# Kernel tuning notes

Hardware: AMD Instinct MI355X
Metric: run time of the kernel (lower is better)

The kernel has to match this reference:

```python
import jax, jax.numpy as jnp
import numpy as np

K = 8
W_CONST = 0.01
EPS = 1e-8


def _normalize(v, eps=1e-8):
    return v / (jnp.linalg.norm(v, axis=-1, keepdims=True) + eps)


def _coarse_normal(x, vertices, vertex_normals):
    # x: (N,3); vertices, vertex_normals: (V,3)
    # brute-force KNN (ascending by squared distance, like cKDTree.query)
    d2_all = jnp.sum((x[:, None, :] - vertices[None, :, :]) ** 2, axis=-1)  # (N,V)
    neg_d2, idx = jax.lax.top_k(-d2_all, K)  # sorted ascending distance
    d2 = -neg_d2                                                    # (N,K)
    v_knn = vertices[idx]                                           # (N,K,3)
    n_knn = vertex_normals[idx]                                     # (N,K,3)
    d2c = jnp.maximum(d2, EPS)
    inv_d2 = 1.0 / d2c                                              # (N,K)
    term_knn = jnp.sum(n_knn * inv_d2[..., None], axis=1)           # (N,3)
    v1 = v_knn[:, 0]                                                # nearest vertex
    d2_v1 = jnp.maximum(jnp.sum((x - v1) ** 2, axis=-1), EPS)       # (N,)
    term_dir = (x - v1) / (W_CONST * d2_v1[:, None])
    W = jnp.sum(inv_d2, axis=1) + 1.0 / W_CONST                     # (N,)
    n_tilde = (term_knn + term_dir) / W[:, None]
    nc = _normalize(n_tilde)
    return nc, v1


def _ray_mesh_first_hit(origins, dirs, tri0, e1, e2):
    # Moller-Trumbore, all points vs all faces. origins/dirs: (N,3); tri0/e1/e2: (F,3)
    pvec = jnp.cross(dirs[:, None, :], e2[None, :, :])              # (N,F,3)
    det = jnp.einsum('fk,nfk->nf', e1, pvec)                        # (N,F)
    ok_det = jnp.abs(det) > EPS
    inv_det = jnp.where(ok_det, 1.0 / jnp.where(ok_det, det, 1.0), 0.0)
    tvec = origins[:, None, :] - tri0[None, :, :]                   # (N,F,3)
    u = jnp.sum(tvec * pvec, axis=-1) * inv_det
    qvec = jnp.cross(tvec, e1[None, :, :])                          # (N,F,3)
    v = jnp.einsum('nk,nfk->nf', dirs, qvec) * inv_det
    t = jnp.einsum('fk,nfk->nf', e2, qvec) * inv_det
    valid = ok_det & (u >= 0.0) & (v >= 0.0) & (u + v <= 1.0) & (t > EPS)
    t_masked = jnp.where(valid, t, jnp.inf)
    t_min = jnp.min(t_masked, axis=1)                               # first hit along ray
    hit = jnp.isfinite(t_min)
    loc = origins + dirs * jnp.where(hit, t_min, 0.0)[:, None]
    return hit, loc


def _project(x, vertices, vertex_normals, faces):
    nc, v1 = _coarse_normal(x, vertices, vertex_normals)
    tri0 = vertices[faces[:, 0]]
    e1 = vertices[faces[:, 1]] - tri0
    e2 = vertices[faces[:, 2]] - tri0
    # primary cast along -nc
    hit1, loc1 = _ray_mesh_first_hit(x, -nc, tri0, e1, e2)
    # fallback cast toward nearest vertex
    dir_fb = _normalize(v1 - x)
    hit2, loc2 = _ray_mesh_first_hit(x, dir_fb, tri0, e1, e2)
    xc = jnp.where(hit1[:, None], loc1, jnp.where(hit2[:, None], loc2, v1))
    s = jnp.sum((x - xc) * nc, axis=-1, keepdims=True)              # (N,1)
    return xc, s, nc


def setup_inputs() -> dict:
    key = jax.random.key(0)
    k1, k2, k3, k4 = jax.random.split(key, 4)
    N, V, F = 2048, 8192, 8192
    x = jax.random.normal(k1, (N, 3), dtype=jnp.float32)
    vertices = jax.random.normal(k2, (V, 3), dtype=jnp.float32)
    vertex_normals = _normalize(jax.random.normal(k3, (V, 3), dtype=jnp.float32))
    faces = jax.random.randint(k4, (F, 3), 0, V, dtype=jnp.int32)
    return {"x": x, "vertices": vertices, "vertex_normals": vertex_normals, "faces": faces}


def reference(x, vertices, vertex_normals, faces):
    # returns (xc:(N,3), s:(N,1), nc:(N,3)) like ProjectionFn.forward
    return _project(x, vertices, vertex_normals, faces)
```

## Files before the change

### kernel.cpp

```cpp
#include <hip/hip_runtime.h>
#include <math.h>

#pragma float_control(precise, on)

#define EPSF 1e-8f


__global__ void __launch_bounds__(256) knn_prep_kernel(
    const float* __restrict__ x, const float* __restrict__ verts,
    const float* __restrict__ vnorm, const int* __restrict__ faces,
    float* __restrict__ tri, float* __restrict__ ncw,
    float* __restrict__ v1w, float* __restrict__ dfbw,
    int N, int V, int F) {
#pragma clang fp contract(off)
    int p = blockIdx.x;
    int tid = threadIdx.x;
    int wave = tid >> 6;
    int lane = tid & 63;
    if (p >= N) return;

    int gt = p * 256 + tid;
    if (gt < F) {
        int f0 = faces[gt * 3 + 0];
        int f1 = faces[gt * 3 + 1];
        int f2 = faces[gt * 3 + 2];
        float t0x = verts[f0 * 3 + 0], t0y = verts[f0 * 3 + 1], t0z = verts[f0 * 3 + 2];
        float ax = verts[f1 * 3 + 0], ay = verts[f1 * 3 + 1], az = verts[f1 * 3 + 2];
        float bx = verts[f2 * 3 + 0], by = verts[f2 * 3 + 1], bz = verts[f2 * 3 + 2];
        float4* t4 = (float4*)(tri + (size_t)gt * 12);
        t4[0] = make_float4(t0x, t0y, t0z, ax - t0x);
        t4[1] = make_float4(ay - t0y, az - t0z, bx - t0x, by - t0y);
        t4[2] = make_float4(bz - t0z, 0.f, 0.f, 0.f);
    }

    float xx = x[p * 3 + 0];
    float xy = x[p * 3 + 1];
    float xz = x[p * 3 + 2];

    unsigned long long ka[8], kb[8];
#pragma unroll
    for (int i = 0; i < 8; ++i) { ka[i] = ~0ULL; kb[i] = ~0ULL; }

    for (int va = tid; va < V; va += 512) {
        int vb = va + 256;
        bool hasB = vb < V;

        float avx = verts[va * 3 + 0];
        float avy = verts[va * 3 + 1];
        float avz = verts[va * 3 + 2];
        float bvx = 0.f, bvy = 0.f, bvz = 0.f;
        if (hasB) {
            bvx = verts[vb * 3 + 0];
            bvy = verts[vb * 3 + 1];
            bvz = verts[vb * 3 + 2];
        }

        float dxa = xx - avx, dya = xy - avy, dza = xz - avz;
        float d2a = ((dxa * dxa) + (dya * dya)) + (dza * dza);
        unsigned long long kA =
            (((unsigned long long)__float_as_uint(d2a)) << 32) | (unsigned int)va;
        if (kA < ka[7]) {
            ka[7] = kA;
#pragma unroll
            for (int j = 7; j > 0; --j) {
                if (ka[j] < ka[j - 1]) {
                    unsigned long long t = ka[j];
                    ka[j] = ka[j - 1];
                    ka[j - 1] = t;
                }
            }
        }

        if (hasB) {
            float dxb = xx - bvx, dyb = xy - bvy, dzb = xz - bvz;
            float d2b = ((dxb * dxb) + (dyb * dyb)) + (dzb * dzb);
            unsigned long long kB =
                (((unsigned long long)__float_as_uint(d2b)) << 32) | (unsigned int)vb;
            if (kB < kb[7]) {
                kb[7] = kB;
#pragma unroll
                for (int j = 7; j > 0; --j) {
                    if (kb[j] < kb[j - 1]) {
                        unsigned long long t = kb[j];
                        kb[j] = kb[j - 1];
                        kb[j - 1] = t;
                    }
                }
            }
        }
    }

    unsigned long long wsel[8];
#pragma unroll
    for (int j = 0; j < 8; ++j) {
        unsigned long long c = (ka[0] < kb[0]) ? ka[0] : kb[0];
        unsigned long long m = c;
#pragma unroll
        for (int s = 1; s < 64; s <<= 1) {
            unsigned long long o = __shfl_xor(m, s, 64);
            if (o < m) m = o;
        }
        if (c == m) {
            if (ka[0] == m) {
#pragma unroll
                for (int t = 0; t < 7; ++t) ka[t] = ka[t + 1];
                ka[7] = ~0ULL;
            } else {
#pragma unroll
                for (int t = 0; t < 7; ++t) kb[t] = kb[t + 1];
                kb[7] = ~0ULL;
            }
        }
        wsel[j] = m;
    }

    __shared__ unsigned long long cand[32];
    if (lane == 0) {
#pragma unroll
        for (int j = 0; j < 8; ++j) cand[wave * 8 + j] = wsel[j];
    }
    __syncthreads();
    if (wave != 0) return;

    unsigned long long c0 = (lane < 32) ? cand[lane] : ~0ULL;
    unsigned long long sel[8];
#pragma unroll
    for (int j = 0; j < 8; ++j) {
        unsigned long long m = c0;
#pragma unroll
        for (int s = 1; s < 64; s <<= 1) {
            unsigned long long o = __shfl_xor(m, s, 64);
            if (o < m) m = o;
        }
        if (c0 == m) c0 = ~0ULL;
        sel[j] = m;
    }

    if (lane != 0) return;

    float invk[8];
    float nsx = 0.f, nsy = 0.f, nsz = 0.f;
#pragma unroll
    for (int j = 0; j < 8; ++j) {
        int id = (int)(sel[j] & 0xffffffffu);
        float d2 = __uint_as_float((unsigned int)(sel[j] >> 32));
        float inv = 1.0f / fmaxf(d2, EPSF);
        invk[j] = inv;
        nsx = nsx + vnorm[id * 3 + 0] * inv;
        nsy = nsy + vnorm[id * 3 + 1] * inv;
        nsz = nsz + vnorm[id * 3 + 2] * inv;
    }
    float Wsum = ((invk[0] + invk[1]) + (invk[2] + invk[3])) +
                 ((invk[4] + invk[5]) + (invk[6] + invk[7]));

    int id0 = (int)(sel[0] & 0xffffffffu);
    float v1x = verts[id0 * 3 + 0];
    float v1y = verts[id0 * 3 + 1];
    float v1z = verts[id0 * 3 + 2];

    float dxv = xx - v1x, dyv = xy - v1y, dzv = xz - v1z;
    float d2v1 = fmaxf(((dxv * dxv) + (dyv * dyv)) + (dzv * dzv), EPSF);
    float den = 0.01f * d2v1;
    float tdx = dxv / den, tdy = dyv / den, tdz = dzv / den;

    float W = Wsum + 100.0f;
    float ntx = (nsx + tdx) / W;
    float nty = (nsy + tdy) / W;
    float ntz = (nsz + tdz) / W;
    float nrm = sqrtf(((ntx * ntx) + (nty * nty)) + (ntz * ntz)) + 1e-8f;
    float ncx = ntx / nrm, ncy = nty / nrm, ncz = ntz / nrm;

    float fx = v1x - xx, fy = v1y - xy, fz = v1z - xz;
    float fn = sqrtf(((fx * fx) + (fy * fy)) + (fz * fz)) + 1e-8f;
    fx = fx / fn; fy = fy / fn; fz = fz / fn;

    ncw[p * 3 + 0] = ncx; ncw[p * 3 + 1] = ncy; ncw[p * 3 + 2] = ncz;
    v1w[p * 3 + 0] = v1x; v1w[p * 3 + 1] = v1y; v1w[p * 3 + 2] = v1z;
    dfbw[p * 3 + 0] = fx; dfbw[p * 3 + 1] = fy; dfbw[p * 3 + 2] = fz;
}

__device__ __forceinline__ float mt_test(
    float ox, float oy, float oz, float dx, float dy, float dz,
    const float4 A, const float4 B, const float4 C, float tb) {
#pragma clang fp contract(off)
    const float M = 1e-5f;
    float e1x = A.w, e1y = B.x, e1z = B.y;
    float e2x = B.z, e2y = B.w, e2z = C.x;
    float tvx = ox - A.x;
    float tvy = oy - A.y;
    float tvz = oz - A.z;
    float qx = (tvy * e1z) - (tvz * e1y);
    float qy = (tvz * e1x) - (tvx * e1z);
    float qz = (tvx * e1y) - (tvy * e1x);
    float tq = ((e2x * qx) + (e2y * qy)) + (e2z * qz);
    float px = (dy * e2z) - (dz * e2y);
    float py = (dz * e2x) - (dx * e2z);
    float pz = (dx * e2y) - (dy * e2x);
    float det = ((e1x * px) + (e1y * py)) + (e1z * pz);
    bool ok = fabsf(det) > EPSF;
    float inv = ok ? (1.0f / det) : 0.0f;
    float u = (((tvx * px) + (tvy * py)) + (tvz * pz)) * inv;
    float v = (((dx * qx) + (dy * qy)) + (dz * qz)) * inv;
    float t = tq * inv;
    bool valid = ok && (u >= -M) && (v >= -M) && ((u + v) <= 1.0f + M) && (t > EPSF);
    return (valid && t < tb) ? t : tb;
}

__global__ void __launch_bounds__(512) ray_fin_kernel(
    const float* __restrict__ x, const float* __restrict__ tri,
    const float* __restrict__ ncw, const float* __restrict__ v1w,
    const float* __restrict__ dfbw, float* __restrict__ out, int N, int F) {
#pragma clang fp contract(off)
    __shared__ unsigned int redA[8], redB[8];
    __shared__ unsigned int u1As, u1Bs, u2As, u2Bs, hAf, hBf;
    int b = blockIdx.x;
    int tid = threadIdx.x;
    int wave = tid >> 6;
    int lane = tid & 63;
    int pA = 2 * b;
    if (pA >= N) return;
    int pB = pA + 1;
    bool hasB = pB < N;
    int pBs = hasB ? pB : pA;

    float axx = x[pA * 3 + 0], axy = x[pA * 3 + 1], axz = x[pA * 3 + 2];
    float Ancx = ncw[pA * 3 + 0], Ancy = ncw[pA * 3 + 1], Ancz = ncw[pA * 3 + 2];
    float Adbx = dfbw[pA * 3 + 0], Adby = dfbw[pA * 3 + 1], Adbz = dfbw[pA * 3 + 2];
    float Adax = -Ancx, Aday = -Ancy, Adaz = -Ancz;

    float bxx = x[pBs * 3 + 0], bxy = x[pBs * 3 + 1], bxz = x[pBs * 3 + 2];
    float Bncx = ncw[pBs * 3 + 0], Bncy = ncw[pBs * 3 + 1], Bncz = ncw[pBs * 3 + 2];
    float Bdbx = dfbw[pBs * 3 + 0], Bdby = dfbw[pBs * 3 + 1], Bdbz = dfbw[pBs * 3 + 2];
    float Bdax = -Bncx, Bday = -Bncy, Bdaz = -Bncz;

    const float INF = __uint_as_float(0x7f800000u);

    float tA = INF, tB = INF;
    for (int fi = tid; fi < F; fi += 512) {
        const float4 A4 = *(const float4*)(tri + (size_t)fi * 12);
        const float4 B4 = *(const float4*)(tri + (size_t)fi * 12 + 4);
        const float4 C4 = *(const float4*)(tri + (size_t)fi * 12 + 8);
        tA = mt_test(axx, axy, axz, Adax, Aday, Adaz, A4, B4, C4, tA);
        tB = mt_test(bxx, bxy, bxz, Bdax, Bday, Bdaz, A4, B4, C4, tB);
    }

    {
        unsigned int ma = __float_as_uint(tA);
        unsigned int mb = __float_as_uint(tB);
#pragma unroll
        for (int s = 1; s < 64; s <<= 1) {
            unsigned int oa = __shfl_xor(ma, s, 64);
            if (oa < ma) ma = oa;
            unsigned int ob = __shfl_xor(mb, s, 64);
            if (ob < mb) mb = ob;
        }
        if (lane == 0) { redA[wave] = ma; redB[wave] = mb; }
    }
    __syncthreads();
    if (tid == 0) {
        unsigned int u1A = min(min(min(redA[0], redA[1]), min(redA[2], redA[3])),
                               min(min(redA[4], redA[5]), min(redA[6], redA[7])));
        unsigned int u1B = min(min(min(redB[0], redB[1]), min(redB[2], redB[3])),
                               min(min(redB[4], redB[5]), min(redB[6], redB[7])));
        u1As = u1A; u1Bs = u1B;
        hAf = (u1A < 0x7f800000u) ? 1u : 0u;
        hBf = (u1B < 0x7f800000u) ? 1u : 0u;
    }
    __syncthreads();

    bool needA = (hAf == 0u);
    bool needB = hasB && (hBf == 0u);
    if (needA || needB) {
        float sA = INF, sB = INF;
        for (int fi = tid; fi < F; fi += 512) {
            const float4 A4 = *(const float4*)(tri + (size_t)fi * 12);
            const float4 B4 = *(const float4*)(tri + (size_t)fi * 12 + 4);
            const float4 C4 = *(const float4*)(tri + (size_t)fi * 12 + 8);
            if (needA) sA = mt_test(axx, axy, axz, Adbx, Adby, Adbz, A4, B4, C4, sA);
            if (needB) sB = mt_test(bxx, bxy, bxz, Bdbx, Bdby, Bdbz, A4, B4, C4, sB);
        }
        unsigned int ma = __float_as_uint(sA);
        unsigned int mb = __float_as_uint(sB);
#pragma unroll
        for (int s = 1; s < 64; s <<= 1) {
            unsigned int oa = __shfl_xor(ma, s, 64);
            if (oa < ma) ma = oa;
            unsigned int ob = __shfl_xor(mb, s, 64);
            if (ob < mb) mb = ob;
        }
        if (lane == 0) { redA[wave] = ma; redB[wave] = mb; }
        __syncthreads();
        if (tid == 0) {
            u2As = min(min(min(redA[0], redA[1]), min(redA[2], redA[3])),
                       min(min(redA[4], redA[5]), min(redA[6], redA[7])));
            u2Bs = min(min(min(redB[0], redB[1]), min(redB[2], redB[3])),
                       min(min(redB[4], redB[5]), min(redB[6], redB[7])));
        }
    }

    if (tid != 0) return;
    {
        float t1 = __uint_as_float(u1As);
        bool h1 = t1 < INF;
        float t2 = h1 ? INF : __uint_as_float(u2As);
        bool h2 = t2 < INF;
        float xcx, xcy, xcz;
        if (h1) {
            xcx = axx + ((-Ancx) * t1);
            xcy = axy + ((-Ancy) * t1);
            xcz = axz + ((-Ancz) * t1);
        } else if (h2) {
            xcx = axx + (Adbx * t2);
            xcy = axy + (Adby * t2);
            xcz = axz + (Adbz * t2);
        } else {
            xcx = v1w[pA * 3 + 0]; xcy = v1w[pA * 3 + 1]; xcz = v1w[pA * 3 + 2];
        }
        float s = (((axx - xcx) * Ancx) + ((axy - xcy) * Ancy)) + ((axz - xcz) * Ancz);
        out[pA * 3 + 0] = xcx;
        out[pA * 3 + 1] = xcy;
        out[pA * 3 + 2] = xcz;
        out[3 * N + pA] = s;
        out[4 * N + pA * 3 + 0] = Ancx;
        out[4 * N + pA * 3 + 1] = Ancy;
        out[4 * N + pA * 3 + 2] = Ancz;
    }
    if (hasB) {
        float t1 = __uint_as_float(u1Bs);
        bool h1 = t1 < INF;
        float t2 = h1 ? INF : __uint_as_float(u2Bs);
        bool h2 = t2 < INF;
        float xcx, xcy, xcz;
        if (h1) {
            xcx = bxx + ((-Bncx) * t1);
            xcy = bxy + ((-Bncy) * t1);
            xcz = bxz + ((-Bncz) * t1);
        } else if (h2) {
            xcx = bxx + (Bdbx * t2);
            xcy = bxy + (Bdby * t2);
            xcz = bxz + (Bdbz * t2);
        } else {
            xcx = v1w[pB * 3 + 0]; xcy = v1w[pB * 3 + 1]; xcz = v1w[pB * 3 + 2];
        }
        float s = (((bxx - xcx) * Bncx) + ((bxy - xcy) * Bncy)) + ((bxz - xcz) * Bncz);
        out[pB * 3 + 0] = xcx;
        out[pB * 3 + 1] = xcy;
        out[pB * 3 + 2] = xcz;
        out[3 * N + pB] = s;
        out[4 * N + pB * 3 + 0] = Bncx;
        out[4 * N + pB * 3 + 1] = Bncy;
        out[4 * N + pB * 3 + 2] = Bncz;
    }
}

extern "C" void kernel_launch(void* const* d_in, const int* in_sizes, int n_in,
                              void* d_out, int out_size, void* d_ws, size_t ws_size,
                              hipStream_t stream) {
    const float* x     = (const float*)d_in[0];
    const float* verts = (const float*)d_in[1];
    const float* vnorm = (const float*)d_in[2];
    const int*   faces = (const int*)d_in[3];
    int N = in_sizes[0] / 3;
    int V = in_sizes[1] / 3;
    int F = in_sizes[3] / 3;

    float* tri  = (float*)d_ws;
    float* ncw  = tri + (size_t)F * 12;
    float* v1w  = ncw + 3 * N;
    float* dfbw = v1w + 3 * N;

    hipLaunchKernelGGL(knn_prep_kernel, dim3(N), dim3(256), 0, stream,
                       x, verts, vnorm, faces, tri, ncw, v1w, dfbw, N, V, F);
    int rblocks = (N + 1) / 2;
    hipLaunchKernelGGL(ray_fin_kernel, dim3(rblocks), dim3(512), 0, stream,
                       x, tri, ncw, v1w, dfbw, (float*)d_out, N, F);
}
```

Measured before the change: 133.4 us.

## Process two query points per KNN block to share vertex loads

The KNN kernel now handles two query points per 512-thread block. Each vertex is loaded once and compared against both points, so each thread keeps two top-8 lists. This halves the global vertex traffic per query and halves the block count, but each thread does two insertions per vertex and the merge now has 8 waves. Triangle precompute becomes a grid-strided loop.

```diff
diff --git a/kernel.cpp b/kernel.cpp
--- a/kernel.cpp
+++ b/kernel.cpp
@@ -6,21 +6,24 @@
 #define EPSF 1e-8f
 
 
-__global__ void __launch_bounds__(256) knn_prep_kernel(
+__global__ void __launch_bounds__(512) knn_prep_kernel(
     const float* __restrict__ x, const float* __restrict__ verts,
     const float* __restrict__ vnorm, const int* __restrict__ faces,
     float* __restrict__ tri, float* __restrict__ ncw,
     float* __restrict__ v1w, float* __restrict__ dfbw,
     int N, int V, int F) {
 #pragma clang fp contract(off)
-    int p = blockIdx.x;
+    int b = blockIdx.x;
     int tid = threadIdx.x;
     int wave = tid >> 6;
     int lane = tid & 63;
-    if (p >= N) return;
-
-    int gt = p * 256 + tid;
-    if (gt < F) {
+    int pA = 2 * b;
+    if (pA >= N) return;
+    int pB = pA + 1;
+    bool hasB = pB < N;
+    int pBs = hasB ? pB : pA;
+
+    for (int gt = b * 512 + tid; gt < F; gt += gridDim.x * 512) {
         int f0 = faces[gt * 3 + 0];
         int f1 = faces[gt * 3 + 1];
         int f2 = faces[gt * 3 + 2];
@@ -33,110 +36,99 @@
         t4[2] = make_float4(bz - t0z, 0.f, 0.f, 0.f);
     }
 
-    float xx = x[p * 3 + 0];
-    float xy = x[p * 3 + 1];
-    float xz = x[p * 3 + 2];
-
-    unsigned long long ka[8], kb[8];
-#pragma unroll
-    for (int i = 0; i < 8; ++i) { ka[i] = ~0ULL; kb[i] = ~0ULL; }
-
-    for (int va = tid; va < V; va += 512) {
-        int vb = va + 256;
-        bool hasB = vb < V;
-
-        float avx = verts[va * 3 + 0];
-        float avy = verts[va * 3 + 1];
-        float avz = verts[va * 3 + 2];
-        float bvx = 0.f, bvy = 0.f, bvz = 0.f;
-        if (hasB) {
-            bvx = verts[vb * 3 + 0];
-            bvy = verts[vb * 3 + 1];
-            bvz = verts[vb * 3 + 2];
-        }
-
-        float dxa = xx - avx, dya = xy - avy, dza = xz - avz;
+    float axx = x[pA * 3 + 0], axy = x[pA * 3 + 1], axz = x[pA * 3 + 2];
+    float bxx = x[pBs * 3 + 0], bxy = x[pBs * 3 + 1], bxz = x[pBs * 3 + 2];
+
+    unsigned long long la[8], lb[8];
+#pragma unroll
+    for (int i = 0; i < 8; ++i) { la[i] = ~0ULL; lb[i] = ~0ULL; }
+
+    for (int v = tid; v < V; v += 512) {
+        float vx = verts[v * 3 + 0];
+        float vy = verts[v * 3 + 1];
+        float vz = verts[v * 3 + 2];
+
+        float dxa = axx - vx, dya = axy - vy, dza = axz - vz;
         float d2a = ((dxa * dxa) + (dya * dya)) + (dza * dza);
         unsigned long long kA =
-            (((unsigned long long)__float_as_uint(d2a)) << 32) | (unsigned int)va;
-        if (kA < ka[7]) {
-            ka[7] = kA;
+            (((unsigned long long)__float_as_uint(d2a)) << 32) | (unsigned int)v;
+        if (kA < la[7]) {
+            la[7] = kA;
 #pragma unroll
             for (int j = 7; j > 0; --j) {
-                if (ka[j] < ka[j - 1]) {
-                    unsigned long long t = ka[j];
-                    ka[j] = ka[j - 1];
-                    ka[j - 1] = t;
+                if (la[j] < la[j - 1]) {
+                    unsigned long long t = la[j];
+                    la[j] = la[j - 1];
+                    la[j - 1] = t;
                 }
             }
         }
 
-        if (hasB) {
-            float dxb = xx - bvx, dyb = xy - bvy, dzb = xz - bvz;
-            float d2b = ((dxb * dxb) + (dyb * dyb)) + (dzb * dzb);
-            unsigned long long kB =
-                (((unsigned long long)__float_as_uint(d2b)) << 32) | (unsigned int)vb;
-            if (kB < kb[7]) {
-                kb[7] = kB;
-#pragma unroll
-                for (int j = 7; j > 0; --j) {
-                    if (kb[j] < kb[j - 1]) {
-                        unsigned long long t = kb[j];
-                        kb[j] = kb[j - 1];
-                        kb[j - 1] = t;
-                    }
+        float dxb = bxx - vx, dyb = bxy - vy, dzb = bxz - vz;
+        float d2b = ((dxb * dxb) + (dyb * dyb)) + (dzb * dzb);
+        unsigned long long kB =
+            (((unsigned long long)__float_as_uint(d2b)) << 32) | (unsigned int)v;
+        if (kB < lb[7]) {
+            lb[7] = kB;
+#pragma unroll
+            for (int j = 7; j > 0; --j) {
+                if (lb[j] < lb[j - 1]) {
+                    unsigned long long t = lb[j];
+                    lb[j] = lb[j - 1];
+                    lb[j - 1] = t;
                 }
             }
         }
     }
 
-    unsigned long long wsel[8];
+    __shared__ unsigned long long candA[64], candB[64];
 #pragma unroll
     for (int j = 0; j < 8; ++j) {
-        unsigned long long c = (ka[0] < kb[0]) ? ka[0] : kb[0];
-        unsigned long long m = c;
+        unsigned long long mA = la[0];
+        unsigned long long mB = lb[0];
+#pragma unroll
+        for (int s = 1; s < 64; s <<= 1) {
+            unsigned long long oA = __shfl_xor(mA, s, 64);
+            if (oA < mA) mA = oA;
+            unsigned long long oB = __shfl_xor(mB, s, 64);
+            if (oB < mB) mB = oB;
+        }
+        if (la[0] == mA) {
+#pragma unroll
+            for (int t = 0; t < 7; ++t) la[t] = la[t + 1];
+            la[7] = ~0ULL;
+        }
+        if (lb[0] == mB) {
+#pragma unroll
+            for (int t = 0; t < 7; ++t) lb[t] = lb[t + 1];
+            lb[7] = ~0ULL;
+        }
+        if (lane == 0) { candA[wave * 8 + j] = mA; candB[wave * 8 + j] = mB; }
+    }
+    __syncthreads();
+
+    if (wave > 1) return;
+    if (wave == 1 && !hasB) return;
+
+    unsigned long long c0 = (wave == 0) ? candA[lane] : candB[lane];
+    unsigned long long sel[8];
+#pragma unroll
+    for (int j = 0; j < 8; ++j) {
+        unsigned long long m = c0;
 #pragma unroll
         for (int s = 1; s < 64; s <<= 1) {
             unsigned long long o = __shfl_xor(m, s, 64);
             if (o < m) m = o;
         }
-        if (c == m) {
-            if (ka[0] == m) {
-#pragma unroll
-                for (int t = 0; t < 7; ++t) ka[t] = ka[t + 1];
-                ka[7] = ~0ULL;
-            } else {
-#pragma unroll
-                for (int t = 0; t < 7; ++t) kb[t] = kb[t + 1];
-                kb[7] = ~0ULL;
-            }
-        }
-        wsel[j] = m;
-    }
-
-    __shared__ unsigned long long cand[32];
-    if (lane == 0) {
-#pragma unroll
-        for (int j = 0; j < 8; ++j) cand[wave * 8 + j] = wsel[j];
-    }
-    __syncthreads();
-    if (wave != 0) return;
-
-    unsigned long long c0 = (lane < 32) ? cand[lane] : ~0ULL;
-    unsigned long long sel[8];
-#pragma unroll
-    for (int j = 0; j < 8; ++j) {
-        unsigned long long m = c0;
-#pragma unroll
-        for (int s = 1; s < 64; s <<= 1) {
-            unsigned long long o = __shfl_xor(m, s, 64);
-            if (o < m) m = o;
-        }
         if (c0 == m) c0 = ~0ULL;
         sel[j] = m;
     }
 
     if (lane != 0) return;
+    int p = (wave == 0) ? pA : pB;
+    float xx = (wave == 0) ? axx : bxx;
+    float xy = (wave == 0) ? axy : bxy;
+    float xz = (wave == 0) ? axz : bxz;
 
     float invk[8];
     float nsx = 0.f, nsy = 0.f, nsz = 0.f;
@@ -369,9 +361,9 @@
     float* v1w  = ncw + 3 * N;
     float* dfbw = v1w + 3 * N;
 
-    hipLaunchKernelGGL(knn_prep_kernel, dim3(N), dim3(256), 0, stream,
+    int pblocks = (N + 1) / 2;
+    hipLaunchKernelGGL(knn_prep_kernel, dim3(pblocks), dim3(512), 0, stream,
                        x, verts, vnorm, faces, tri, ncw, v1w, dfbw, N, V, F);
-    int rblocks = (N + 1) / 2;
-    hipLaunchKernelGGL(ray_fin_kernel, dim3(rblocks), dim3(512), 0, stream,
+    hipLaunchKernelGGL(ray_fin_kernel, dim3(pblocks), dim3(512), 0, stream,
                        x, tri, ncw, v1w, dfbw, (float*)d_out, N, F);
 }
```

New measurement: 135.6 us. No clear change (+1.7%).
